# Kernel optimization log

Measured on AMD Instinct MI355X. Metric: run time of the kernel, lower is better.

## Reference

```python
import jax, jax.numpy as jnp
import numpy as np

N_NODES = 50000
N_EDGES = 800000
D_IN = 96
D_OUT = 96
N_GRAPHS = 50


def setup_inputs() -> dict:
    key = jax.random.key(0)
    ks = jax.random.split(key, 16)
    s = 1.0 / np.sqrt(D_IN)
    inp = {
        "x": jax.random.normal(ks[0], (N_NODES, D_IN), jnp.float32),
        "edge_index": jax.random.randint(ks[1], (2, N_EDGES), 0, N_NODES, jnp.int32),
        "edge_attr": jax.random.uniform(ks[2], (N_EDGES, 1), jnp.float32),
        "batch": jnp.sort(jax.random.randint(ks[3], (N_NODES,), 0, N_GRAPHS, jnp.int32)),
        "w1_w": jax.random.normal(ks[4], (D_IN, D_OUT), jnp.float32) * s,
        "w1_b": jax.random.normal(ks[5], (D_OUT,), jnp.float32) * 0.01,
        "w2_w": jax.random.normal(ks[6], (D_IN, D_OUT), jnp.float32) * s,
        "w2_b": jax.random.normal(ks[7], (D_OUT,), jnp.float32) * 0.01,
        "w3_w": jax.random.normal(ks[8], (D_IN, D_OUT), jnp.float32) * s,
        "w3_b": jax.random.normal(ks[9], (D_OUT,), jnp.float32) * 0.01,
        "w4_w": jax.random.normal(ks[10], (D_IN, D_OUT), jnp.float32) * s,
        "w4_b": jax.random.normal(ks[11], (D_OUT,), jnp.float32) * 0.01,
        "w5_w": jax.random.normal(ks[12], (1, D_OUT), jnp.float32),
        "w5_b": jax.random.normal(ks[13], (D_OUT,), jnp.float32) * 0.01,
    }
    return inp


def reference(x, edge_index, edge_attr, batch,
              w1_w, w1_b, w2_w, w2_b, w3_w, w3_b, w4_w, w4_b, w5_w, w5_b):
    n = x.shape[0]
    src, dst = edge_index[0], edge_index[1]  # x_j = x[src], x_i = x[dst]
    sqrt_d = jnp.sqrt(jnp.asarray(D_OUT, x.dtype))

    x_i = x[dst]                                  # [E, D]
    x_j = x[src]                                  # [E, D]
    xi_t = x_i @ w3_w + w3_b                      # w3(x_i)
    xj_t = x_j @ w4_w + w4_b                      # w4(x_j)
    ea_t = edge_attr @ w5_w + w5_b                # w5(edge_attr), [E, D]

    scores = jnp.sum(xi_t * (xj_t + ea_t), axis=-1) / sqrt_d  # [E]

    # segment softmax over destination-node neighborhoods (PyG softmax)
    seg_max = jax.ops.segment_max(scores, dst, num_segments=n)
    ex = jnp.exp(scores - seg_max[dst])
    denom = jax.ops.segment_sum(ex, dst, num_segments=n)
    alpha = ex / (denom[dst] + jnp.asarray(1e-16, x.dtype))

    msg = alpha[:, None] * (x_j @ w2_w + w2_b)    # [E, D]
    aggr = jax.ops.segment_sum(msg, dst, num_segments=n)

    node_out = x @ w1_w + w1_b + aggr             # update: w1(x) + aggr

    # global mean pool per graph
    sums = jax.ops.segment_sum(node_out, batch, num_segments=N_GRAPHS)
    counts = jax.ops.segment_sum(jnp.ones((n,), x.dtype), batch, num_segments=N_GRAPHS)
    return sums / jnp.maximum(counts, 1.0)[:, None]
```

## Files before the change

kernel.cpp:

```cpp
#include <hip/hip_runtime.h>
#include <math.h>

#define D 96
#define RSQ 0.10206207261596577f

typedef __attribute__((ext_vector_type(8))) short short8;
typedef __attribute__((ext_vector_type(4))) float f32x4;

__device__ __forceinline__ unsigned short f2bf(float f){
  unsigned u = __float_as_uint(f);
  unsigned r = (u + 0x7fff + ((u >> 16) & 1)) >> 16;
  return (unsigned short)r;
}
__device__ __forceinline__ float bf2f(unsigned short h){
  return __uint_as_float(((unsigned)h) << 16);
}
__device__ __forceinline__ float bflo(unsigned u){ return __uint_as_float(u << 16); }
__device__ __forceinline__ float bfhi(unsigned u){ return __uint_as_float(u & 0xffff0000u); }
__device__ __forceinline__ int lbound(const int* __restrict__ a, int n, int v){
  int lo = 0, hi = n;
  while (lo < hi){ int mid = (lo + hi) >> 1; if (a[mid] < v) lo = mid + 1; else hi = mid; }
  return lo;
}

__global__ __launch_bounds__(256) void k_wprep_deg(
    const float* __restrict__ w1, const float* __restrict__ w2,
    const float* __restrict__ w3, const float* __restrict__ w4,
    unsigned short* __restrict__ wt_h, unsigned short* __restrict__ wt_l,
    const int* __restrict__ dstI, int* __restrict__ deg,
    int* __restrict__ rank, int E){
  int gtid = blockIdx.x * 256 + threadIdx.x;
  if (gtid < 4 * D * D){
    int m = gtid / (D * D);
    int r = gtid % (D * D);
    int nn = r / D, k = r % D;
    const float* w = (m == 0) ? w1 : (m == 1) ? w2 : (m == 2) ? w3 : w4;
    float v = w[k * D + nn];
    unsigned short h = f2bf(v);
    wt_h[gtid] = h;
    wt_l[gtid] = f2bf(v - bf2f(h));
  }
  if (gtid < E) rank[gtid] = atomicAdd(&deg[dstI[gtid]], 1);
}

__global__ __launch_bounds__(256) void k_transform_mfma(
    const float* __restrict__ x,
    const unsigned short* __restrict__ wt_h, const unsigned short* __restrict__ wt_l,
    const float* __restrict__ b1, const float* __restrict__ b2,
    const float* __restrict__ b3, const float* __restrict__ b4,
    const float* __restrict__ w5, const float* __restrict__ b5,
    float* __restrict__ acc_o, unsigned short* __restrict__ x24,
    float* __restrict__ x3o,
    float* __restrict__ p5, float* __restrict__ pb, int n, int NT){
  __shared__ __align__(16) unsigned short wlds[4][2][D * D];
  __shared__ __align__(16) unsigned short xs_h[16][104];
  __shared__ __align__(16) unsigned short xs_l[16][104];
  int tid = threadIdx.x;

  {
    const short8* gh = (const short8*)wt_h;
    const short8* gl = (const short8*)wt_l;
    for (int c = tid; c < 4 * D * D / 8; c += 256){
      int m = c / (D * D / 8);
      int r = c - m * (D * D / 8);
      *(short8*)&wlds[m][0][r * 8] = gh[c];
      *(short8*)&wlds[m][1][r * 8] = gl[c];
    }
  }

  int wv = tid >> 6;
  int lane = tid & 63, lr = lane & 15, kg = lane >> 4;
  const unsigned short* Wh = &wlds[wv][0][0];
  const unsigned short* Wl = &wlds[wv][1][0];
  const float* bias = (wv == 0) ? b1 : (wv == 1) ? b2 : (wv == 2) ? b3 : b4;

  for (int tile = blockIdx.x; tile < NT; tile += gridDim.x){
    int n0 = tile * 16;
    __syncthreads();
    for (int e = tid; e < 16 * D; e += 256){
      int r = e / D, cc = e % D;
      int node = n0 + r;
      float v = (node < n) ? x[(size_t)node * D + cc] : 0.0f;
      unsigned short h = f2bf(v);
      xs_h[r][cc] = h;
      xs_l[r][cc] = f2bf(v - bf2f(h));
    }
    __syncthreads();

    f32x4 acc[6];
    #pragma unroll
    for (int i = 0; i < 6; ++i) acc[i] = (f32x4){0, 0, 0, 0};
    #pragma unroll
    for (int k0i = 0; k0i < 3; ++k0i){
      int kb = k0i * 32 + kg * 8;
      short8 ah = *(const short8*)&xs_h[lr][kb];
      short8 al = *(const short8*)&xs_l[lr][kb];
      #pragma unroll
      for (int nc = 0; nc < 6; ++nc){
        int col = nc * 16 + lr;
        short8 bh = *(const short8*)(Wh + col * D + kb);
        short8 bl = *(const short8*)(Wl + col * D + kb);
        acc[nc] = __builtin_amdgcn_mfma_f32_16x16x32_bf16(ah, bh, acc[nc], 0, 0, 0);
        acc[nc] = __builtin_amdgcn_mfma_f32_16x16x32_bf16(ah, bl, acc[nc], 0, 0, 0);
        acc[nc] = __builtin_amdgcn_mfma_f32_16x16x32_bf16(al, bh, acc[nc], 0, 0, 0);
      }
    }

    f32x4 p5a = {0, 0, 0, 0}, pba = {0, 0, 0, 0};
    #pragma unroll
    for (int nc = 0; nc < 6; ++nc){
      int col = nc * 16 + lr;
      float bb = bias[col];
      float w5v = w5[col], b5v = b5[col];
      #pragma unroll
      for (int q = 0; q < 4; ++q){
        float v = acc[nc][q] + bb;
        int row = kg * 4 + q;
        if (n0 + row < n){
          if (wv == 0) acc_o[(size_t)(n0 + row) * D + col] = v;
          else if (wv == 1) x24[(size_t)(n0 + row) * 192 + 96 + col] = f2bf(v);
          else if (wv == 2) x3o[(size_t)(n0 + row) * D + col] = v;
          else x24[(size_t)(n0 + row) * 192 + col] = f2bf(v);
        }
        p5a[q] += v * w5v;
        pba[q] += v * b5v;
      }
    }
    if (wv == 2){
      #pragma unroll
      for (int off = 1; off < 16; off <<= 1){
        #pragma unroll
        for (int q = 0; q < 4; ++q){
          p5a[q] += __shfl_xor(p5a[q], off);
          pba[q] += __shfl_xor(pba[q], off);
        }
      }
      if (lr == 0){
        #pragma unroll
        for (int q = 0; q < 4; ++q){
          int row = kg * 4 + q;
          if (n0 + row < n){ p5[n0 + row] = p5a[q]; pb[n0 + row] = pba[q]; }
        }
      }
    }
  }
}

__global__ __launch_bounds__(256) void k_scanA(
    const int* __restrict__ deg, int* __restrict__ rowp,
    int* __restrict__ partials, int n){
  __shared__ int ws[4];
  int tid = threadIdx.x, lane = tid & 63, wid = tid >> 6;
  int i = blockIdx.x * 256 + tid;
  int v = (i < n) ? deg[i] : 0;
  int s = v;
  #pragma unroll
  for (int off = 1; off < 64; off <<= 1){ int u = __shfl_up(s, off); if (lane >= off) s += u; }
  if (lane == 63) ws[wid] = s;
  __syncthreads();
  if (tid < 4){
    int u = ws[tid];
    #pragma unroll
    for (int off = 1; off < 4; off <<= 1){ int q = __shfl_up(u, off); if (tid >= off) u += q; }
    ws[tid] = u;
  }
  __syncthreads();
  int woff = wid ? ws[wid - 1] : 0;
  if (i < n) rowp[i] = woff + s - v;
  if (tid == 255) partials[blockIdx.x] = ws[3];
}

__global__ __launch_bounds__(256) void k_scanB(
    int* __restrict__ partials, int* __restrict__ rowp, int nb, int n){
  __shared__ int ws[4];
  int tid = threadIdx.x, lane = tid & 63, wid = tid >> 6;
  int running = 0;
  for (int base = 0; base < nb; base += 256){
    int i = base + tid;
    int v = (i < nb) ? partials[i] : 0;
    int s = v;
    #pragma unroll
    for (int off = 1; off < 64; off <<= 1){ int u = __shfl_up(s, off); if (lane >= off) s += u; }
    if (lane == 63) ws[wid] = s;
    __syncthreads();
    if (tid < 4){
      int u = ws[tid];
      #pragma unroll
      for (int off = 1; off < 4; off <<= 1){ int q = __shfl_up(u, off); if (tid >= off) u += q; }
      ws[tid] = u;
    }
    __syncthreads();
    int woff = wid ? ws[wid - 1] : 0;
    if (i < nb) partials[i] = running + woff + s - v;
    running += ws[3];
    __syncthreads();
  }
  if (tid == 0) rowp[n] = running;
}

__global__ __launch_bounds__(256) void k_scatter(
    const int* __restrict__ srcI, const int* __restrict__ dstI,
    const float* __restrict__ eattr, const int* __restrict__ rowp,
    const int* __restrict__ partials, const int* __restrict__ rank,
    int2* __restrict__ sortedSE, int E){
  int e = blockIdx.x * blockDim.x + threadIdx.x;
  if (e >= E) return;
  int t = dstI[e];
  int pos = rowp[t] + partials[t >> 8] + rank[e];
  sortedSE[pos] = make_int2(srcI[e], __float_as_int(eattr[e]));
}

__global__ __launch_bounds__(256) void k_attn(
    const unsigned short* __restrict__ x24, const float* __restrict__ x3,
    const float* __restrict__ p5,
    const float* __restrict__ pb, const int2* __restrict__ sortedSE,
    const int* __restrict__ rowp, const int* __restrict__ partials,
    float* __restrict__ node_acc, int n){
  int t = blockIdx.x * 4 + (threadIdx.x >> 6);
  int lane = threadIdx.x & 63;
  if (t >= n) return;
  int beg = rowp[t] + partials[t >> 8];
  int end = (t + 1 < n) ? (rowp[t + 1] + partials[(t + 1) >> 8]) : rowp[n];
  if (beg == end) return;
  int j = lane & 15;
  int g = lane >> 4;

  const float2* r3 = (const float2*)(x3 + (size_t)t * D);
  float2 v0 = r3[j], v1 = r3[j + 16], v2 = r3[j + 32];
  float p5t = p5[t], pbt = pb[t];

  float m = -INFINITY, dsum = 0.0f;
  float a0 = 0, a1 = 0, a2 = 0, a3 = 0, a4 = 0, a5 = 0;

  for (int c = beg; c < end; c += 8){
    int eA = c + g, eB = c + 4 + g;
    bool actA = eA < end, actB = eB < end;
    int2 seA = sortedSE[actA ? eA : end - 1];
    int2 seB = sortedSE[actB ? eB : end - 1];
    const unsigned* rA = (const unsigned*)(x24 + (size_t)seA.x * 192);
    const unsigned* rB = (const unsigned*)(x24 + (size_t)seB.x * 192);
    unsigned uA0 = rA[j], uA1 = rA[j + 16], uA2 = rA[j + 32];
    unsigned uB0 = rB[j], uB1 = rB[j + 16], uB2 = rB[j + 32];
    float sA = v0.x * bflo(uA0) + v0.y * bfhi(uA0)
             + v1.x * bflo(uA1) + v1.y * bfhi(uA1)
             + v2.x * bflo(uA2) + v2.y * bfhi(uA2);
    float sB = v0.x * bflo(uB0) + v0.y * bfhi(uB0)
             + v1.x * bflo(uB1) + v1.y * bfhi(uB1)
             + v2.x * bflo(uB2) + v2.y * bfhi(uB2);
    sA += __shfl_xor(sA, 1); sA += __shfl_xor(sA, 2);
    sA += __shfl_xor(sA, 4); sA += __shfl_xor(sA, 8);
    sB += __shfl_xor(sB, 1); sB += __shfl_xor(sB, 2);
    sB += __shfl_xor(sB, 4); sB += __shfl_xor(sB, 8);
    float scA = actA ? (sA + __int_as_float(seA.y) * p5t + pbt) * RSQ : -INFINITY;
    float scB = actB ? (sB + __int_as_float(seB.y) * p5t + pbt) * RSQ : -INFINITY;
    float mc = fmaxf(scA, scB);
    mc = fmaxf(mc, __shfl_xor(mc, 16));
    mc = fmaxf(mc, __shfl_xor(mc, 32));
    if (mc > m){
      float r = __expf(m - mc);
      dsum *= r; a0 *= r; a1 *= r; a2 *= r; a3 *= r; a4 *= r; a5 *= r;
      m = mc;
    }
    float wA = __expf(scA - m);
    float wB = __expf(scB - m);
    dsum += wA + wB;
    unsigned qA0 = rA[48 + j], qA1 = rA[48 + j + 16], qA2 = rA[48 + j + 32];
    unsigned qB0 = rB[48 + j], qB1 = rB[48 + j + 16], qB2 = rB[48 + j + 32];
    a0 += wA * bflo(qA0) + wB * bflo(qB0);
    a1 += wA * bfhi(qA0) + wB * bfhi(qB0);
    a2 += wA * bflo(qA1) + wB * bflo(qB1);
    a3 += wA * bfhi(qA1) + wB * bfhi(qB1);
    a4 += wA * bflo(qA2) + wB * bflo(qB2);
    a5 += wA * bfhi(qA2) + wB * bfhi(qB2);
  }
  a0 += __shfl_xor(a0, 16); a0 += __shfl_xor(a0, 32);
  a1 += __shfl_xor(a1, 16); a1 += __shfl_xor(a1, 32);
  a2 += __shfl_xor(a2, 16); a2 += __shfl_xor(a2, 32);
  a3 += __shfl_xor(a3, 16); a3 += __shfl_xor(a3, 32);
  a4 += __shfl_xor(a4, 16); a4 += __shfl_xor(a4, 32);
  a5 += __shfl_xor(a5, 16); a5 += __shfl_xor(a5, 32);
  dsum += __shfl_xor(dsum, 16); dsum += __shfl_xor(dsum, 32);
  float inv = 1.0f / (dsum + 1e-16f);
  if (lane < 16){
    size_t o = (size_t)t * D + 2 * j;
    node_acc[o]      += a0 * inv;
    node_acc[o + 1]  += a1 * inv;
    node_acc[o + 32] += a2 * inv;
    node_acc[o + 33] += a3 * inv;
    node_acc[o + 64] += a4 * inv;
    node_acc[o + 65] += a5 * inv;
  }
}

__global__ __launch_bounds__(96) void k_pool(
    const float* __restrict__ node_out, const int* __restrict__ batch,
    float* __restrict__ sums, int n){
  int g = blockIdx.x;
  int chunk = blockIdx.y, nch = gridDim.y;
  int lo = lbound(batch, n, g);
  int hi = lbound(batch, n, g + 1);
  int cnt = hi - lo;
  if (cnt <= 0) return;
  int per = (cnt + nch - 1) / nch;
  int b = lo + chunk * per;
  int e = min(b + per, hi);
  if (b >= e) return;
  int d = threadIdx.x;
  float s = 0.0f;
  for (int r = b; r < e; ++r) s += node_out[(size_t)r * D + d];
  atomicAdd(&sums[g * D + d], s);
}

__global__ __launch_bounds__(256) void k_final(
    const float* __restrict__ sums, const int* __restrict__ batch,
    float* __restrict__ out, int n, int total){
  int i = blockIdx.x * blockDim.x + threadIdx.x;
  if (i >= total) return;
  int g = i / D;
  int lo = lbound(batch, n, g);
  int hi = lbound(batch, n, g + 1);
  float c = (float)((hi - lo) > 1 ? (hi - lo) : 1);
  out[i] = sums[i] / c;
}

extern "C" void kernel_launch(void* const* d_in, const int* in_sizes, int n_in,
                              void* d_out, int out_size, void* d_ws, size_t ws_size,
                              hipStream_t stream){
  const float* x     = (const float*)d_in[0];
  const int*   eidx  = (const int*)d_in[1];
  const float* eattr = (const float*)d_in[2];
  const int*   batch = (const int*)d_in[3];
  const float* w1 = (const float*)d_in[4];
  const float* b1 = (const float*)d_in[5];
  const float* w2 = (const float*)d_in[6];
  const float* b2 = (const float*)d_in[7];
  const float* w3 = (const float*)d_in[8];
  const float* b3 = (const float*)d_in[9];
  const float* w4 = (const float*)d_in[10];
  const float* b4 = (const float*)d_in[11];
  const float* w5 = (const float*)d_in[12];
  const float* b5 = (const float*)d_in[13];
  float* out = (float*)d_out;

  const int N = in_sizes[0] / D;
  const int E = in_sizes[2];
  const int* srcI = eidx;
  const int* dstI = eidx + E;
  const int NB = (N + 255) / 256;
  const int NT = (N + 15) / 16;
  const int TGRID = (NT < 256) ? NT : 256;

  char* base = (char*)d_ws;
  size_t off = 0;
  auto alloc = [&](size_t bytes) -> char* {
    char* p = base + off;
    off = (off + bytes + 255) & ~(size_t)255;
    return p;
  };
  char* zbase = base;
  int*   deg   = (int*)alloc((size_t)N * 4);
  float* sums  = (float*)alloc((size_t)out_size * 4);
  size_t zbytes = off;
  float* node_acc = (float*)alloc((size_t)N * D * 4);
  unsigned short* x24 = (unsigned short*)alloc((size_t)N * 192 * 2);
  float* x3v      = (float*)alloc((size_t)N * D * 4);
  float* p5       = (float*)alloc((size_t)N * 4);
  float* pb       = (float*)alloc((size_t)N * 4);
  int*   rowp     = (int*)alloc((size_t)(N + 1) * 4);
  int*   partials = (int*)alloc((size_t)(NB + 1) * 4);
  int*   rank     = (int*)alloc((size_t)E * 4);
  int2*  sortedSE = (int2*)alloc((size_t)E * 8);
  unsigned short* wt_h = (unsigned short*)alloc((size_t)4 * D * D * 2);
  unsigned short* wt_l = (unsigned short*)alloc((size_t)4 * D * D * 2);
  (void)ws_size; (void)n_in;

  hipMemsetAsync(zbase, 0, zbytes, stream);

  k_wprep_deg<<<dim3((E + 255) / 256), dim3(256), 0, stream>>>(
      w1, w2, w3, w4, wt_h, wt_l, dstI, deg, rank, E);
  k_transform_mfma<<<dim3(TGRID), dim3(256), 0, stream>>>(
      x, wt_h, wt_l, b1, b2, b3, b4, w5, b5,
      node_acc, x24, x3v, p5, pb, N, NT);
  k_scanA<<<dim3(NB), dim3(256), 0, stream>>>(deg, rowp, partials, N);
  k_scanB<<<dim3(1), dim3(256), 0, stream>>>(partials, rowp, NB, N);
  k_scatter<<<dim3((E + 255) / 256), dim3(256), 0, stream>>>(
      srcI, dstI, eattr, rowp, partials, rank, sortedSE, E);
  k_attn<<<dim3((N + 3) / 4), dim3(256), 0, stream>>>(
      x24, x3v, p5, pb, sortedSE, rowp, partials, node_acc, N);
  k_pool<<<dim3(out_size / D, 32), dim3(D), 0, stream>>>(node_acc, batch, sums, N);
  k_final<<<dim3((out_size + 255) / 256), dim3(256), 0, stream>>>(
      sums, batch, out, N, out_size);
}
```

Baseline: 308.9 us.

## Drop LDS weight staging; one tile per block reading weights from global

The transform kernel no longer copies all four split-bf16 weight matrices (about 147KB) into LDS at block start, and no longer loops persistently over tiles. Each block now handles a single 16-node tile, the grid grows to one block per tile, and B fragments are loaded straight from global memory (expected to hit in L2 or L1), issued up front for all six column chunks. This removes the large LDS footprint, which limited occupancy to one block per CU, and the per-block weight preload. In exchange every block re-reads weights from the cache hierarchy and pays more block launch overhead.

Result: faster. 267.7 us (-13.3%).

```diff
diff --git a/kernel.cpp b/kernel.cpp
--- a/kernel.cpp
+++ b/kernel.cpp
@@ -51,96 +51,105 @@
     const float* __restrict__ w5, const float* __restrict__ b5,
     float* __restrict__ acc_o, unsigned short* __restrict__ x24,
     float* __restrict__ x3o,
-    float* __restrict__ p5, float* __restrict__ pb, int n, int NT){
-  __shared__ __align__(16) unsigned short wlds[4][2][D * D];
+    float* __restrict__ p5, float* __restrict__ pb, int n){
   __shared__ __align__(16) unsigned short xs_h[16][104];
   __shared__ __align__(16) unsigned short xs_l[16][104];
   int tid = threadIdx.x;
-
-  {
-    const short8* gh = (const short8*)wt_h;
-    const short8* gl = (const short8*)wt_l;
-    for (int c = tid; c < 4 * D * D / 8; c += 256){
-      int m = c / (D * D / 8);
-      int r = c - m * (D * D / 8);
-      *(short8*)&wlds[m][0][r * 8] = gh[c];
-      *(short8*)&wlds[m][1][r * 8] = gl[c];
-    }
-  }
+  int n0 = blockIdx.x * 16;
+  for (int e = tid; e < 16 * D; e += 256){
+    int r = e / D, c = e % D;
+    int node = n0 + r;
+    float v = (node < n) ? x[(size_t)node * D + c] : 0.0f;
+    unsigned short h = f2bf(v);
+    xs_h[r][c] = h;
+    xs_l[r][c] = f2bf(v - bf2f(h));
+  }
+  __syncthreads();
 
   int wv = tid >> 6;
   int lane = tid & 63, lr = lane & 15, kg = lane >> 4;
-  const unsigned short* Wh = &wlds[wv][0][0];
-  const unsigned short* Wl = &wlds[wv][1][0];
+  const unsigned short* Wh = wt_h + (size_t)wv * D * D;
+  const unsigned short* Wl = wt_l + (size_t)wv * D * D;
+
+  f32x4 acc0 = {0,0,0,0}, acc1 = {0,0,0,0}, acc2 = {0,0,0,0};
+  f32x4 acc3 = {0,0,0,0}, acc4 = {0,0,0,0}, acc5 = {0,0,0,0};
+
+  #pragma unroll
+  for (int k0i = 0; k0i < 3; ++k0i){
+    int kb = k0i * 32 + kg * 8;
+    short8 ah = *(const short8*)&xs_h[lr][kb];
+    short8 al = *(const short8*)&xs_l[lr][kb];
+    const unsigned short* bp = Wh + lr * D + kb;
+    const unsigned short* lp = Wl + lr * D + kb;
+    short8 bh0 = *(const short8*)(bp);
+    short8 bh1 = *(const short8*)(bp + 16 * D);
+    short8 bh2 = *(const short8*)(bp + 32 * D);
+    short8 bh3 = *(const short8*)(bp + 48 * D);
+    short8 bh4 = *(const short8*)(bp + 64 * D);
+    short8 bh5 = *(const short8*)(bp + 80 * D);
+    short8 bl0 = *(const short8*)(lp);
+    short8 bl1 = *(const short8*)(lp + 16 * D);
+    short8 bl2 = *(const short8*)(lp + 32 * D);
+    short8 bl3 = *(const short8*)(lp + 48 * D);
+    short8 bl4 = *(const short8*)(lp + 64 * D);
+    short8 bl5 = *(const short8*)(lp + 80 * D);
+    acc0 = __builtin_amdgcn_mfma_f32_16x16x32_bf16(ah, bh0, acc0, 0, 0, 0);
+    acc0 = __builtin_amdgcn_mfma_f32_16x16x32_bf16(ah, bl0, acc0, 0, 0, 0);
+    acc0 = __builtin_amdgcn_mfma_f32_16x16x32_bf16(al, bh0, acc0, 0, 0, 0);
+    acc1 = __builtin_amdgcn_mfma_f32_16x16x32_bf16(ah, bh1, acc1, 0, 0, 0);
+    acc1 = __builtin_amdgcn_mfma_f32_16x16x32_bf16(ah, bl1, acc1, 0, 0, 0);
+    acc1 = __builtin_amdgcn_mfma_f32_16x16x32_bf16(al, bh1, acc1, 0, 0, 0);
+    acc2 = __builtin_amdgcn_mfma_f32_16x16x32_bf16(ah, bh2, acc2, 0, 0, 0);
+    acc2 = __builtin_amdgcn_mfma_f32_16x16x32_bf16(ah, bl2, acc2, 0, 0, 0);
+    acc2 = __builtin_amdgcn_mfma_f32_16x16x32_bf16(al, bh2, acc2, 0, 0, 0);
+    acc3 = __builtin_amdgcn_mfma_f32_16x16x32_bf16(ah, bh3, acc3, 0, 0, 0);
+    acc3 = __builtin_amdgcn_mfma_f32_16x16x32_bf16(ah, bl3, acc3, 0, 0, 0);
+    acc3 = __builtin_amdgcn_mfma_f32_16x16x32_bf16(al, bh3, acc3, 0, 0, 0);
+    acc4 = __builtin_amdgcn_mfma_f32_16x16x32_bf16(ah, bh4, acc4, 0, 0, 0);
+    acc4 = __builtin_amdgcn_mfma_f32_16x16x32_bf16(ah, bl4, acc4, 0, 0, 0);
+    acc4 = __builtin_amdgcn_mfma_f32_16x16x32_bf16(al, bh4, acc4, 0, 0, 0);
+    acc5 = __builtin_amdgcn_mfma_f32_16x16x32_bf16(ah, bh5, acc5, 0, 0, 0);
+    acc5 = __builtin_amdgcn_mfma_f32_16x16x32_bf16(ah, bl5, acc5, 0, 0, 0);
+    acc5 = __builtin_amdgcn_mfma_f32_16x16x32_bf16(al, bh5, acc5, 0, 0, 0);
+  }
+
   const float* bias = (wv == 0) ? b1 : (wv == 1) ? b2 : (wv == 2) ? b3 : b4;
-
-  for (int tile = blockIdx.x; tile < NT; tile += gridDim.x){
-    int n0 = tile * 16;
-    __syncthreads();
-    for (int e = tid; e < 16 * D; e += 256){
-      int r = e / D, cc = e % D;
-      int node = n0 + r;
-      float v = (node < n) ? x[(size_t)node * D + cc] : 0.0f;
-      unsigned short h = f2bf(v);
-      xs_h[r][cc] = h;
-      xs_l[r][cc] = f2bf(v - bf2f(h));
-    }
-    __syncthreads();
-
-    f32x4 acc[6];
+  f32x4 p5a = {0, 0, 0, 0}, pba = {0, 0, 0, 0};
+  #define EPI_BODY(nc, C) { \
+    int col = (nc) * 16 + lr; \
+    float bb = bias[col]; \
+    float w5v = w5[col], b5v = b5[col]; \
+    _Pragma("unroll") \
+    for (int q = 0; q < 4; ++q){ \
+      float v = C[q] + bb; \
+      int row = kg * 4 + q; \
+      if (n0 + row < n){ \
+        if (wv == 0) acc_o[(size_t)(n0 + row) * D + col] = v; \
+        else if (wv == 1) x24[(size_t)(n0 + row) * 192 + 96 + col] = f2bf(v); \
+        else if (wv == 2) x3o[(size_t)(n0 + row) * D + col] = v; \
+        else x24[(size_t)(n0 + row) * 192 + col] = f2bf(v); \
+      } \
+      p5a[q] += v * w5v; \
+      pba[q] += v * b5v; \
+    } }
+  EPI_BODY(0, acc0) EPI_BODY(1, acc1) EPI_BODY(2, acc2)
+  EPI_BODY(3, acc3) EPI_BODY(4, acc4) EPI_BODY(5, acc5)
+  #undef EPI_BODY
+
+  if (wv == 2){
     #pragma unroll
-    for (int i = 0; i < 6; ++i) acc[i] = (f32x4){0, 0, 0, 0};
-    #pragma unroll
-    for (int k0i = 0; k0i < 3; ++k0i){
-      int kb = k0i * 32 + kg * 8;
-      short8 ah = *(const short8*)&xs_h[lr][kb];
-      short8 al = *(const short8*)&xs_l[lr][kb];
+    for (int off = 1; off < 16; off <<= 1){
       #pragma unroll
-      for (int nc = 0; nc < 6; ++nc){
-        int col = nc * 16 + lr;
-        short8 bh = *(const short8*)(Wh + col * D + kb);
-        short8 bl = *(const short8*)(Wl + col * D + kb);
-        acc[nc] = __builtin_amdgcn_mfma_f32_16x16x32_bf16(ah, bh, acc[nc], 0, 0, 0);
-        acc[nc] = __builtin_amdgcn_mfma_f32_16x16x32_bf16(ah, bl, acc[nc], 0, 0, 0);
-        acc[nc] = __builtin_amdgcn_mfma_f32_16x16x32_bf16(al, bh, acc[nc], 0, 0, 0);
+      for (int q = 0; q < 4; ++q){
+        p5a[q] += __shfl_xor(p5a[q], off);
+        pba[q] += __shfl_xor(pba[q], off);
       }
     }
-
-    f32x4 p5a = {0, 0, 0, 0}, pba = {0, 0, 0, 0};
-    #pragma unroll
-    for (int nc = 0; nc < 6; ++nc){
-      int col = nc * 16 + lr;
-      float bb = bias[col];
-      float w5v = w5[col], b5v = b5[col];
+    if (lr == 0){
       #pragma unroll
       for (int q = 0; q < 4; ++q){
-        float v = acc[nc][q] + bb;
         int row = kg * 4 + q;
-        if (n0 + row < n){
-          if (wv == 0) acc_o[(size_t)(n0 + row) * D + col] = v;
-          else if (wv == 1) x24[(size_t)(n0 + row) * 192 + 96 + col] = f2bf(v);
-          else if (wv == 2) x3o[(size_t)(n0 + row) * D + col] = v;
-          else x24[(size_t)(n0 + row) * 192 + col] = f2bf(v);
-        }
-        p5a[q] += v * w5v;
-        pba[q] += v * b5v;
-      }
-    }
-    if (wv == 2){
-      #pragma unroll
-      for (int off = 1; off < 16; off <<= 1){
-        #pragma unroll
-        for (int q = 0; q < 4; ++q){
-          p5a[q] += __shfl_xor(p5a[q], off);
-          pba[q] += __shfl_xor(pba[q], off);
-        }
-      }
-      if (lr == 0){
-        #pragma unroll
-        for (int q = 0; q < 4; ++q){
-          int row = kg * 4 + q;
-          if (n0 + row < n){ p5[n0 + row] = p5a[q]; pb[n0 + row] = pba[q]; }
-        }
+        if (n0 + row < n){ p5[n0 + row] = p5a[q]; pb[n0 + row] = pba[q]; }
       }
     }
   }
@@ -348,7 +357,6 @@
   const int* dstI = eidx + E;
   const int NB = (N + 255) / 256;
   const int NT = (N + 15) / 16;
-  const int TGRID = (NT < 256) ? NT : 256;
 
   char* base = (char*)d_ws;
   size_t off = 0;
@@ -378,9 +386,9 @@
 
   k_wprep_deg<<<dim3((E + 255) / 256), dim3(256), 0, stream>>>(
       w1, w2, w3, w4, wt_h, wt_l, dstI, deg, rank, E);
-  k_transform_mfma<<<dim3(TGRID), dim3(256), 0, stream>>>(
+  k_transform_mfma<<<dim3(NT), dim3(256), 0, stream>>>(
       x, wt_h, wt_l, b1, b2, b3, b4, w5, b5,
-      node_acc, x24, x3v, p5, pb, N, NT);
+      node_acc, x24, x3v, p5, pb, N);
   k_scanA<<<dim3(NB), dim3(256), 0, stream>>>(deg, rowp, partials, N);
   k_scanB<<<dim3(1), dim3(256), 0, stream>>>(partials, rowp, NB, N);
   k_scatter<<<dim3((E + 255) / 256), dim3(256), 0, stream>>>(
```
